# Kernel tuning notes

Hardware: AMD Instinct MI355X
Metric: run time of the kernel (lower is better)

The kernel has to match this reference:

```python
import jax, jax.numpy as jnp
import numpy as np

V, E, H, C = 30000, 128, 256, 9  # vocab, embed dim, lstm hidden, num tags
B, S = 64, 512


def setup_inputs() -> dict:
    key = jax.random.key(0)
    ks = jax.random.split(key, 16)
    rn = lambda k, shape: jax.random.normal(k, shape, jnp.float32) * 0.1
    return {
        "token_ids": jax.random.randint(ks[0], (B, S), 0, V),
        "labels": jax.random.randint(ks[1], (B, S), 0, C),
        "attention_masks": jnp.ones((B, S), jnp.int32),
        "emb": rn(ks[2], (V, E)),
        # layer 0: input E; layer 1: input 2H. dim 0 = direction (fwd, bwd)
        "w_ih0": rn(ks[3], (2, 4 * H, E)),
        "w_hh0": rn(ks[4], (2, 4 * H, H)),
        "b_ih0": rn(ks[5], (2, 4 * H)),
        "b_hh0": rn(ks[6], (2, 4 * H)),
        "w_ih1": rn(ks[7], (2, 4 * H, 2 * H)),
        "w_hh1": rn(ks[8], (2, 4 * H, H)),
        "b_ih1": rn(ks[9], (2, 4 * H)),
        "b_hh1": rn(ks[10], (2, 4 * H)),
        "cls_w": rn(ks[11], (C, 2 * H)),
        "cls_b": rn(ks[12], (C,)),
        "start_trans": rn(ks[13], (C,)),
        "end_trans": rn(ks[14], (C,)),
        "trans": rn(ks[15], (C, C)),
    }


def _lstm_dir(x, w_ih, w_hh, b_ih, b_hh, reverse):
    # x: [B,S,in] -> [B,S,H]; gate order i,f,g,o as in torch
    Bq = x.shape[0]
    Hq = w_hh.shape[1]
    xg = jnp.einsum('bsi,gi->bsg', x, w_ih) + b_ih  # [B,S,4H]

    def step(carry, xg_t):
        h, c = carry
        g = xg_t + h @ w_hh.T + b_hh
        i, f, gg, o = jnp.split(g, 4, axis=-1)
        c = jax.nn.sigmoid(f) * c + jax.nn.sigmoid(i) * jnp.tanh(gg)
        h = jax.nn.sigmoid(o) * jnp.tanh(c)
        return (h, c), h

    init = (jnp.zeros((Bq, Hq), x.dtype), jnp.zeros((Bq, Hq), x.dtype))
    _, hs = jax.lax.scan(step, init, jnp.swapaxes(xg, 0, 1), reverse=reverse)
    return jnp.swapaxes(hs, 0, 1)


def _bilstm_layer(x, w_ih, w_hh, b_ih, b_hh):
    fwd = _lstm_dir(x, w_ih[0], w_hh[0], b_ih[0], b_hh[0], False)
    bwd = _lstm_dir(x, w_ih[1], w_hh[1], b_ih[1], b_hh[1], True)
    return jnp.concatenate([fwd, bwd], axis=-1)


def _crf_llh(em, tags, mask, start, end, trans):
    # torchcrf log-likelihood; em [B,S,C], tags [B,S], mask [B,S]
    m = mask.astype(em.dtype)
    em_tag = jnp.take_along_axis(em, tags[..., None], axis=2)[..., 0]  # [B,S]
    tr = trans[tags[:, :-1], tags[:, 1:]]  # [B,S-1]
    num = start[tags[:, 0]] + em_tag[:, 0] + jnp.sum(m[:, 1:] * (tr + em_tag[:, 1:]), axis=1)
    last_idx = jnp.sum(mask, axis=1).astype(jnp.int32) - 1
    last_tag = jnp.take_along_axis(tags, last_idx[:, None], axis=1)[:, 0]
    num = num + end[last_tag]

    alpha0 = start[None, :] + em[:, 0]  # [B,C]

    def step(alpha, xs):
        em_t, m_t = xs
        nxt = jax.nn.logsumexp(alpha[:, :, None] + trans[None] + em_t[:, None, :], axis=1)
        return jnp.where(m_t[:, None] > 0, nxt, alpha), None

    xs = (jnp.swapaxes(em[:, 1:], 0, 1), jnp.swapaxes(m[:, 1:], 0, 1))
    alpha, _ = jax.lax.scan(step, alpha0, xs)
    den = jax.nn.logsumexp(alpha + end[None, :], axis=1)
    return num - den


def _viterbi(em, mask, start, end, trans):
    Cq = em.shape[2]
    m = mask > 0
    score0 = start[None, :] + em[:, 0]
    idc = jnp.arange(Cq, dtype=jnp.int32)

    def step(score, xs):
        em_t, m_t = xs
        brd = score[:, :, None] + trans[None]  # [B,C_prev,C_next]
        best_prev = jnp.argmax(brd, axis=1).astype(jnp.int32)
        nxt = jnp.max(brd, axis=1) + em_t
        new = jnp.where(m_t[:, None], nxt, score)
        bp = jnp.where(m_t[:, None], best_prev, idc[None, :])  # self-pointer past seq end
        return new, bp

    xs = (jnp.swapaxes(em[:, 1:], 0, 1), jnp.swapaxes(m[:, 1:], 0, 1))
    score, hist = jax.lax.scan(step, score0, xs)  # hist: [S-1,B,C]
    last = jnp.argmax(score + end[None, :], axis=1).astype(jnp.int32)

    def back(tag, bp_t):
        prev = jnp.take_along_axis(bp_t, tag[:, None], axis=1)[:, 0]
        return prev, prev

    _, prevs = jax.lax.scan(back, last, hist, reverse=True)  # [S-1,B]
    return jnp.concatenate([jnp.swapaxes(prevs, 0, 1), last[:, None]], axis=1)  # [B,S]


def reference(token_ids, labels, attention_masks, emb, w_ih0, w_hh0, b_ih0, b_hh0,
              w_ih1, w_hh1, b_ih1, b_hh1, cls_w, cls_b, start_trans, end_trans, trans):
    x = emb[token_ids]  # [B,S,E]
    h = _bilstm_layer(x, w_ih0, w_hh0, b_ih0, b_hh0)  # [B,S,2H] (eval mode: no dropout)
    h = _bilstm_layer(h, w_ih1, w_hh1, b_ih1, b_hh1)
    emissions = h @ cls_w.T + cls_b  # [B,S,C]
    llh = _crf_llh(emissions, labels, attention_masks, start_trans, end_trans, trans)
    loss = -jnp.mean(llh)  # reduction='mean', negated
    tags = _viterbi(emissions, attention_masks, start_trans, end_trans, trans)
    return (loss, tags)
```

## Files before the change

kernel.cpp:

```cpp
#include <hip/hip_runtime.h>
#include <math.h>

#define BB 64
#define SS 512
#define EE 128
#define HH 256
#define NC 9
#define G4 1024
#define TCLOG 7
#define TC 128
#define NCH (SS / TC)

#define KLQ 9

typedef _Float16 half2v __attribute__((ext_vector_type(2)));

__device__ __forceinline__ float sigf(float x) {
    return 1.0f / (1.0f + __expf(-x));
}
__device__ __forceinline__ float tanhfast(float x) {
    float a = fabsf(x);
    float e = __expf(-2.0f * a);
    float t = (1.0f - e) / (1.0f + e);
    return copysignf(t, x);
}
__device__ __forceinline__ float dot8h(uint4 w, uint4 h, float acc) {
    acc = __builtin_amdgcn_fdot2(__builtin_bit_cast(half2v, w.x),
                                 __builtin_bit_cast(half2v, h.x), acc, false);
    acc = __builtin_amdgcn_fdot2(__builtin_bit_cast(half2v, w.y),
                                 __builtin_bit_cast(half2v, h.y), acc, false);
    acc = __builtin_amdgcn_fdot2(__builtin_bit_cast(half2v, w.z),
                                 __builtin_bit_cast(half2v, h.z), acc, false);
    acc = __builtin_amdgcn_fdot2(__builtin_bit_cast(half2v, w.w),
                                 __builtin_bit_cast(half2v, h.w), acc, false);
    return acc;
}
__device__ __forceinline__ int dot16q(uint4 w, uint4 h, int acc) {
    acc = __builtin_amdgcn_sdot4((int)w.x, (int)h.x, acc, false);
    acc = __builtin_amdgcn_sdot4((int)w.y, (int)h.y, acc, false);
    acc = __builtin_amdgcn_sdot4((int)w.z, (int)h.z, acc, false);
    acc = __builtin_amdgcn_sdot4((int)w.w, (int)h.w, acc, false);
    return acc;
}
__device__ __forceinline__ ushort f16b(float x) {
    return __builtin_bit_cast(ushort, (_Float16)x);
}

__global__ void quant_whh(const float* __restrict__ whh, uint* __restrict__ wTq,
                          float* __restrict__ swf) {
    const int row = blockIdx.x;
    const int t = threadIdx.x;
    float4 v = *(const float4*)(whh + (long)row * 256 + t * 4);
    float mx = fmaxf(fmaxf(fabsf(v.x), fabsf(v.y)), fmaxf(fabsf(v.z), fabsf(v.w)));
    #pragma unroll
    for (int o = 32; o > 0; o >>= 1) mx = fmaxf(mx, __shfl_xor(mx, o));
    float inv = (mx > 0.f) ? 127.f / mx : 0.f;
    int q0 = (int)rintf(v.x * inv) & 255;
    int q1 = (int)rintf(v.y * inv) & 255;
    int q2 = (int)rintf(v.z * inv) & 255;
    int q3 = (int)rintf(v.w * inv) & 255;
    uint u = (uint)q0 | ((uint)q1 << 8) | ((uint)q2 << 16) | ((uint)q3 << 24);
    const int dir = row >> 10, j = row & 1023;
    const int kc = t >> 2, l4 = t & 3;
    wTq[(((long)(dir * 16 + kc) * 1024 + j) << 2) + l4] = u;
    if (t == 0) swf[row] = (mx > 0.f) ? (mx / 127.f) * (1.f / 127.f) : 0.f;
}

__global__ void quant_wih1(const float* __restrict__ w, uint* __restrict__ wq,
                           float* __restrict__ swf) {
    const int row = blockIdx.x;
    const int t = threadIdx.x;
    float4 a = *(const float4*)(w + (long)row * 512 + t * 8);
    float4 b = *(const float4*)(w + (long)row * 512 + t * 8 + 4);
    float mx = fmaxf(fmaxf(fmaxf(fabsf(a.x), fabsf(a.y)), fmaxf(fabsf(a.z), fabsf(a.w))),
                     fmaxf(fmaxf(fabsf(b.x), fabsf(b.y)), fmaxf(fabsf(b.z), fabsf(b.w))));
    #pragma unroll
    for (int o = 32; o > 0; o >>= 1) mx = fmaxf(mx, __shfl_xor(mx, o));
    float inv = (mx > 0.f) ? 127.f / mx : 0.f;
    uint q0 = (uint)((int)rintf(a.x * inv) & 255) | ((uint)((int)rintf(a.y * inv) & 255) << 8)
            | ((uint)((int)rintf(a.z * inv) & 255) << 16) | ((uint)((int)rintf(a.w * inv) & 255) << 24);
    uint q1 = (uint)((int)rintf(b.x * inv) & 255) | ((uint)((int)rintf(b.y * inv) & 255) << 8)
            | ((uint)((int)rintf(b.z * inv) & 255) << 16) | ((uint)((int)rintf(b.w * inv) & 255) << 24);
    wq[(long)row * 128 + t * 2]     = q0;
    wq[(long)row * 128 + t * 2 + 1] = q1;
    if (t == 0) swf[row] = (mx > 0.f) ? mx / (127.f * 127.f) : 0.f;
}

__global__ void pack_f16(const float* __restrict__ in, ushort* __restrict__ out, int n8) {
    int i = blockIdx.x * 256 + threadIdx.x;
    if (i >= n8) return;
    float4 a = *(const float4*)(in + (long)i * 8);
    float4 b = *(const float4*)(in + (long)i * 8 + 4);
    _Float16 o[8] = {(_Float16)a.x, (_Float16)a.y, (_Float16)a.z, (_Float16)a.w,
                     (_Float16)b.x, (_Float16)b.y, (_Float16)b.z, (_Float16)b.w};
    *(uint4*)(out + (long)i * 8) = *(uint4*)o;
}

template <int KDIM, bool GATHER>
__global__ __launch_bounds__(256, 2) void gemm_xg16b(
    const void* __restrict__ Av, const int* __restrict__ tokens,
    const ushort* __restrict__ Wh, const float* __restrict__ bias,
    float* __restrict__ out, int t_base, int t_sign)
{
    __shared__ uint4 As[2][144];
    __shared__ uint4 Bs[2][144];
    const int tid = threadIdx.x;
    const int m0 = blockIdx.x * 128;
    const int n0 = blockIdx.y * 128;

    const int lr  = tid & 127;
    const int lk8 = tid >> 7;
    const int tcc = (m0 + lr) & (TC - 1);
    const int b   = (m0 + lr) >> TCLOG;
    const int tglob = t_base + t_sign * tcc;
    const long arow = (long)b * SS + tglob;
    const float*  Af = GATHER ? ((const float*)Av + (long)tokens[arow] * KDIM + lk8 * 8) : nullptr;
    const ushort* Ah = GATHER ? nullptr : ((const ushort*)Av + arow * (long)KDIM + lk8 * 8);
    const ushort* Wp = Wh + (long)(n0 + lr) * KDIM + lk8 * 8;
    const int lpad = lr + (lr >> 3);

    const int tr = tid >> 4;
    const int tn = tid & 15;

    float acc[8][8];
    #pragma unroll
    for (int i = 0; i < 8; i++)
        #pragma unroll
        for (int j = 0; j < 8; j++) acc[i][j] = 0.f;

    #pragma unroll 1
    for (int k0 = 0; k0 < KDIM; k0 += 16) {
        uint4 aw, bw;
        if (GATHER) {
            float4 a0 = *(const float4*)(Af + k0);
            float4 a1 = *(const float4*)(Af + k0 + 4);
            aw.x = (uint)f16b(a0.x) | ((uint)f16b(a0.y) << 16);
            aw.y = (uint)f16b(a0.z) | ((uint)f16b(a0.w) << 16);
            aw.z = (uint)f16b(a1.x) | ((uint)f16b(a1.y) << 16);
            aw.w = (uint)f16b(a1.z) | ((uint)f16b(a1.w) << 16);
        } else {
            aw = *(const uint4*)(Ah + k0);
        }
        bw = *(const uint4*)(Wp + k0);
        As[lk8][lpad] = aw;
        Bs[lk8][lpad] = bw;
        __syncthreads();
        #pragma unroll
        for (int k8 = 0; k8 < 2; k8++) {
            uint4 a[8], w[8];
            #pragma unroll
            for (int i = 0; i < 8; i++) {
                a[i] = As[k8][tr * 9 + i];
                w[i] = Bs[k8][tn * 9 + i];
            }
            #pragma unroll
            for (int i = 0; i < 8; i++)
                #pragma unroll
                for (int j = 0; j < 8; j++)
                    acc[i][j] = dot8h(w[j], a[i], acc[i][j]);
        }
        __syncthreads();
    }

    float4 bc0 = *(const float4*)(bias + n0 + tn * 8);
    float4 bc1 = *(const float4*)(bias + n0 + tn * 8 + 4);
    #pragma unroll
    for (int i = 0; i < 8; i++) {
        float* op = out + (long)(m0 + tr * 8 + i) * G4 + n0 + tn * 8;
        float4 r0, r1;
        r0.x = acc[i][0] + bc0.x; r0.y = acc[i][1] + bc0.y;
        r0.z = acc[i][2] + bc0.z; r0.w = acc[i][3] + bc0.w;
        r1.x = acc[i][4] + bc1.x; r1.y = acc[i][5] + bc1.y;
        r1.z = acc[i][6] + bc1.z; r1.w = acc[i][7] + bc1.w;
        *(float4*)op = r0;
        *(float4*)(op + 4) = r1;
    }
}

__global__ __launch_bounds__(256, 2) void gemm_xg8(
    const unsigned char* __restrict__ A8,
    const uint* __restrict__ Wq,
    const float* __restrict__ swf,
    const float* __restrict__ bias,
    float* __restrict__ out,
    int t_base, int t_sign)
{
    __shared__ uint4 As[144];
    __shared__ uint4 Bs[144];
    const int tid = threadIdx.x;
    const int m0 = blockIdx.x * 128;
    const int n0 = blockIdx.y * 128;

    const int lr   = tid & 127;
    const int half = tid >> 7;
    const int tcc = (m0 + lr) & (TC - 1);
    const int b   = (m0 + lr) >> TCLOG;
    const int tglob = t_base + t_sign * tcc;
    const long arow = (long)b * SS + tglob;
    const uint4* Ap = (const uint4*)(A8 + arow * 512);
    const uint4* Wp = (const uint4*)Wq + (long)(n0 + lr) * 32;
    const int lpad = lr + (lr >> 3);

    const int tr = tid >> 4;
    const int tn = tid & 15;

    int acc[8][8];
    #pragma unroll
    for (int i = 0; i < 8; i++)
        #pragma unroll
        for (int j = 0; j < 8; j++) acc[i][j] = 0;

    #pragma unroll 1
    for (int k0 = 0; k0 < 32; k0++) {
        uint4 v = half ? Wp[k0] : Ap[k0];
        if (half) Bs[lpad] = v; else As[lpad] = v;
        __syncthreads();
        uint4 a[8], w[8];
        #pragma unroll
        for (int i = 0; i < 8; i++) {
            a[i] = As[tr * 9 + i];
            w[i] = Bs[tn * 9 + i];
        }
        #pragma unroll
        for (int i = 0; i < 8; i++)
            #pragma unroll
            for (int j = 0; j < 8; j++)
                acc[i][j] = dot16q(w[j], a[i], acc[i][j]);
        __syncthreads();
    }

    float s[8], bs[8];
    #pragma unroll
    for (int jj = 0; jj < 8; jj++) {
        s[jj]  = swf[n0 + tn * 8 + jj];
        bs[jj] = bias[n0 + tn * 8 + jj];
    }
    #pragma unroll
    for (int i = 0; i < 8; i++) {
        float r[8];
        #pragma unroll
        for (int jj = 0; jj < 8; jj++) r[jj] = fmaf((float)acc[i][jj], s[jj], bs[jj]);
        float* op = out + (long)(m0 + tr * 8 + i) * G4 + n0 + tn * 8;
        *(float4*)op       = make_float4(r[0], r[1], r[2], r[3]);
        *(float4*)(op + 4) = make_float4(r[4], r[5], r[6], r[7]);
    }
}

__global__ __launch_bounds__(1024, 4) void lstm_qscan(
    const float* __restrict__ xgF, const float* __restrict__ xgB,
    const uint* __restrict__ wTq,
    const float* __restrict__ swf,
    const float* __restrict__ bhh2,
    ushort* __restrict__ hout,
    unsigned char* __restrict__ hout8,
    int doW8,
    float* __restrict__ state,
    int tbF, int tbB, int doInit)
{
    const int b = blockIdx.x;
    const int d = blockIdx.y;
    const int j = threadIdx.x;
    const float* xg = (d ? xgB : xgF) + (long)b * TC * G4 + j;
    const uint4* wTd = (const uint4*)wTq + (long)d * 16 * 1024;

    __shared__ __align__(16) uint hq[2][64];
    __shared__ float gl[G4];
    __shared__ uint4 lwq[KLQ * 1024];

    #pragma unroll
    for (int kc = 0; kc < KLQ; kc++)
        lwq[kc * 1024 + j] = wTd[(long)kc * 1024 + j];

    const float bj  = bhh2[d * G4 + j];
    const float scl = swf[d * G4 + j];
    float c_reg = 0.f, h_reg = 0.f;
    if (j < HH) {
        if (!doInit) {
            h_reg = state[((d * BB + b) * 2 + 0) * HH + j];
            c_reg = state[((d * BB + b) * 2 + 1) * HH + j];
        }
        ((char*)hq[0])[j] = (char)__float2int_rn(h_reg * 127.f);
    }
    __syncthreads();

    #pragma unroll 1
    for (int tc = 0; tc < TC; ++tc) {
        const int rb = tc & 1;
        const uint4* hc = (const uint4*)hq[rb];
        int isum = 0;

        #pragma unroll
        for (int kc = 0; kc < KLQ; kc++)
            isum = dot16q(lwq[kc * 1024 + j], hc[kc], isum);
        #pragma unroll
        for (int kc = KLQ; kc < 16; kc++)
            isum = dot16q(wTd[(long)kc * 1024 + j], hc[kc], isum);

        gl[j] = fmaf((float)isum, scl, xg[(long)tc * G4] + bj);
        __syncthreads();
        if (j < HH) {
            float gi = gl[j], gf = gl[j + 256], gg = gl[j + 512], go = gl[j + 768];
            c_reg = sigf(gf) * c_reg + sigf(gi) * tanhfast(gg);
            float h = sigf(go) * tanhfast(c_reg);
            h_reg = h;
            int qh = __float2int_rn(h * 127.f);
            ((char*)hq[rb ^ 1])[j] = (char)qh;
            const int t = d ? (tbB - tc) : (tbF + tc);
            if (doW8) hout8[((long)(b * SS + t)) * 512 + d * HH + j] = (unsigned char)(char)qh;
            else      hout [((long)(b * SS + t)) * 512 + d * HH + j] = f16b(h);
        }
        __syncthreads();
    }

    if (j < HH) {
        state[((d * BB + b) * 2 + 0) * HH + j] = h_reg;
        state[((d * BB + b) * 2 + 1) * HH + j] = c_reg;
    }
}

__global__ __launch_bounds__(256) void emissions_k16(
    const ushort* __restrict__ h1, const float* __restrict__ clsw,
    const float* __restrict__ clsb, float* __restrict__ em)
{
    long u = (long)blockIdx.x * 256 + threadIdx.x;
    if (u >= (long)BB * SS * NC) return;
    int c = (int)(u % NC);
    long m = u / NC;
    const uint* hr = (const uint*)(h1 + m * 512);
    const float2* wr = (const float2*)(clsw + (long)c * 512);
    float s0 = 0, s1 = 0;
    #pragma unroll 8
    for (int q = 0; q < 256; q += 2) {
        half2v h0 = __builtin_bit_cast(half2v, hr[q]);
        half2v h1v = __builtin_bit_cast(half2v, hr[q + 1]);
        float2 w0 = wr[q], w1 = wr[q + 1];
        s0 += (float)h0.x * w0.x + (float)h0.y * w0.y;
        s1 += (float)h1v.x * w1.x + (float)h1v.y * w1.y;
    }
    em[u] = s0 + s1 + clsb[c];
}

__global__ __launch_bounds__(64) void crf_llh(
    const float* __restrict__ em, const int* __restrict__ labels,
    const int* __restrict__ mask, const float* __restrict__ start,
    const float* __restrict__ endt, const float* __restrict__ trans,
    float* __restrict__ llh)
{
    int b = blockIdx.x, j = threadIdx.x;
    bool act = j < NC;
    float tcol[NC];
    #pragma unroll
    for (int i = 0; i < NC; i++) tcol[i] = act ? trans[i * NC + j] : 0.f;
    const float* emb_ = em + (long)b * SS * NC;
    const int* lb = labels + b * SS;
    const int* mk = mask + b * SS;
    float alpha = act ? (start[j] + emb_[j]) : -1e30f;

    float num = 0.f;
    int msum = 0;
    for (int t = j; t < SS; t += 64) msum += (mk[t] != 0);
    for (int t = 1 + j; t < SS; t += 64) {
        float m = (float)mk[t];
        num += m * (trans[lb[t - 1] * NC + lb[t]] + emb_[t * NC + lb[t]]);
    }
    for (int o = 32; o > 0; o >>= 1) {
        num  += __shfl_down(num, o);
        msum += __shfl_down(msum, o);
    }
    msum = __shfl(msum, 0);

    for (int t = 1; t < SS; t++) {
        int m = mk[t];
        float emj = act ? emb_[t * NC + j] : 0.f;
        float v[NC];
        float mx = -1e30f;
        #pragma unroll
        for (int i = 0; i < NC; i++) {
            v[i] = __shfl(alpha, i) + tcol[i];
            mx = fmaxf(mx, v[i]);
        }
        float sum = 0.f;
        #pragma unroll
        for (int i = 0; i < NC; i++) sum += __expf(v[i] - mx);
        float nxt = mx + __logf(sum) + emj;
        if (m > 0 && act) alpha = nxt;
    }
    float fin = act ? alpha + endt[j] : -1e30f;
    float mx = -1e30f;
    #pragma unroll
    for (int i = 0; i < NC; i++) mx = fmaxf(mx, __shfl(fin, i));
    float s = 0.f;
    #pragma unroll
    for (int i = 0; i < NC; i++) s += __expf(__shfl(fin, i) - mx);
    float den = mx + __logf(s);
    if (j == 0) {
        int last_idx = msum - 1;
        float numer = num + start[lb[0]] + emb_[lb[0]] + endt[lb[last_idx]];
        llh[b] = numer - den;
    }
}

__global__ __launch_bounds__(64) void loss_k(const float* __restrict__ llh, float* __restrict__ out) {
    int j = threadIdx.x;
    float v = llh[j];
    for (int o = 32; o > 0; o >>= 1) v += __shfl_down(v, o);
    if (j == 0) out[0] = -v / 64.0f;
}

__global__ __launch_bounds__(64) void viterbi_k(
    const float* __restrict__ em, const int* __restrict__ mask,
    const float* __restrict__ start, const float* __restrict__ endt,
    const float* __restrict__ trans, float* __restrict__ outp)
{
    int b = blockIdx.x, j = threadIdx.x;
    bool act = j < NC;
    __shared__ unsigned char bp[SS][NC];
    float tcol[NC];
    #pragma unroll
    for (int i = 0; i < NC; i++) tcol[i] = act ? trans[i * NC + j] : 0.f;
    const float* emb_ = em + (long)b * SS * NC;
    const int* mk = mask + b * SS;
    float score = act ? (start[j] + emb_[j]) : -1e30f;

    for (int t = 1; t < SS; t++) {
        float best = 0.f;
        int bi = 0;
        #pragma unroll
        for (int i = 0; i < NC; i++) {
            float vv = __shfl(score, i) + tcol[i];
            if (i == 0 || vv > best) { best = vv; bi = i; }
        }
        int m = mk[t];
        float nxt = best + (act ? emb_[t * NC + j] : 0.f);
        if (act) {
            if (m > 0) { score = nxt; bp[t][j] = (unsigned char)bi; }
            else       { bp[t][j] = (unsigned char)j; }
        }
    }
    float fin = act ? score + endt[j] : -1e30f;
    float bestf = 0.f;
    int last = 0;
    #pragma unroll
    for (int i = 0; i < NC; i++) {
        float vv = __shfl(fin, i);
        if (i == 0 || vv > bestf) { bestf = vv; last = i; }
    }
    __syncthreads();
    if (j == 0) {
        int cur = last;
        outp[1 + (long)b * SS + (SS - 1)] = (float)cur;
        for (int t = SS - 1; t >= 1; t--) {
            cur = bp[t][cur];
            outp[1 + (long)b * SS + (t - 1)] = (float)cur;
        }
    }
}

extern "C" void kernel_launch(void* const* d_in, const int* in_sizes, int n_in,
                              void* d_out, int out_size, void* d_ws, size_t ws_size,
                              hipStream_t stream) {
    const int*   tok    = (const int*)d_in[0];
    const int*   lab    = (const int*)d_in[1];
    const int*   msk    = (const int*)d_in[2];
    const float* emb    = (const float*)d_in[3];
    const float* w_ih0  = (const float*)d_in[4];
    const float* w_hh0  = (const float*)d_in[5];
    const float* b_ih0  = (const float*)d_in[6];
    const float* b_hh0  = (const float*)d_in[7];
    const float* w_ih1  = (const float*)d_in[8];
    const float* w_hh1  = (const float*)d_in[9];
    const float* b_ih1  = (const float*)d_in[10];
    const float* b_hh1  = (const float*)d_in[11];
    const float* clsw   = (const float*)d_in[12];
    const float* clsb   = (const float*)d_in[13];
    const float* startt = (const float*)d_in[14];
    const float* endt   = (const float*)d_in[15];
    const float* transm = (const float*)d_in[16];
    float* out = (float*)d_out;

    size_t nH8  = (size_t)BB * SS * 512 / 4;
    size_t nHh  = (size_t)BB * SS * 512 / 2;
    size_t nWQ  = (size_t)2 * 16 * 1024 * 4;
    size_t nSW  = (size_t)2 * 1024;
    size_t nWI0 = (size_t)2048 * 128 / 2;
    size_t nWQ1 = (size_t)2048 * 128;
    size_t nEM  = (size_t)BB * SS * NC;
    size_t nST  = (size_t)2 * BB * 2 * HH;
    size_t nXG  = (size_t)BB * TC * G4;

    float* H08f = (float*)d_ws;
    float* H1f  = H08f + nH8;
    float* WQ0  = H1f + nHh;
    float* WQ1w = WQ0 + nWQ;
    float* SW0  = WQ1w + nWQ;
    float* SW1  = SW0 + nSW;
    float* WI0  = SW1 + nSW;
    float* WQI1 = WI0 + nWI0;
    float* SWI1 = WQI1 + nWQ1;
    float* EM   = SWI1 + 2048;
    float* ST   = EM + nEM;
    float* LLH  = ST + nST;
    float* XGF  = LLH + 64;
    float* XGB  = XGF + nXG;

    unsigned char* H08 = (unsigned char*)H08f;
    ushort* H1h  = (ushort*)H1f;
    ushort* WI0h = (ushort*)WI0;

    quant_whh<<<2048, 64, 0, stream>>>(w_hh0, (uint*)WQ0, SW0);
    quant_whh<<<2048, 64, 0, stream>>>(w_hh1, (uint*)WQ1w, SW1);
    quant_wih1<<<2048, 64, 0, stream>>>(w_ih1, (uint*)WQI1, SWI1);
    pack_f16<<<(2048 * 128 / 8 + 255) / 256, 256, 0, stream>>>(w_ih0, WI0h, 2048 * 128 / 8);

    dim3 gg2((BB * TC) / 128, G4 / 128);
    dim3 rg(BB, 2);

    for (int c = 0; c < NCH; c++) {
        int tbF = c * TC;
        int tbB = SS - 1 - c * TC;
        gemm_xg16b<128, true><<<gg2, 256, 0, stream>>>(emb, tok, WI0h,              b_ih0,        XGF, tbF, +1);
        gemm_xg16b<128, true><<<gg2, 256, 0, stream>>>(emb, tok, WI0h + 1024 * 128, b_ih0 + 1024, XGB, tbB, -1);
        lstm_qscan<<<rg, 1024, 0, stream>>>(XGF, XGB, (const uint*)WQ0, SW0, b_hh0,
                                            H1h, H08, 1, ST, tbF, tbB, c == 0);
    }
    for (int c = 0; c < NCH; c++) {
        int tbF = c * TC;
        int tbB = SS - 1 - c * TC;
        gemm_xg8<<<gg2, 256, 0, stream>>>(H08, (const uint*)WQI1,              SWI1,        b_ih1,        XGF, tbF, +1);
        gemm_xg8<<<gg2, 256, 0, stream>>>(H08, (const uint*)WQI1 + 1024 * 128, SWI1 + 1024, b_ih1 + 1024, XGB, tbB, -1);
        lstm_qscan<<<rg, 1024, 0, stream>>>(XGF, XGB, (const uint*)WQ1w, SW1, b_hh1,
                                            H1h, H08, 0, ST, tbF, tbB, c == 0);
    }

    emissions_k16<<<((BB * SS * NC) + 255) / 256, 256, 0, stream>>>(H1h, clsw, clsb, EM);
    crf_llh<<<BB, 64, 0, stream>>>(EM, lab, msk, startt, endt, transm, LLH);
    loss_k<<<1, 64, 0, stream>>>(LLH, out);
    viterbi_k<<<BB, 64, 0, stream>>>(EM, msk, startt, endt, transm, out);
}
```

Measured before the change: 2.249 ms.

## Fuse LSTM scan and next-chunk input GEMMs into one overlapped megakernel

New measurement: 2.195 ms. 1.02x faster.

```diff
diff --git a/kernel.cpp b/kernel.cpp
--- a/kernel.cpp
+++ b/kernel.cpp
@@ -3,7 +3,6 @@
 
 #define BB 64
 #define SS 512
-#define EE 128
 #define HH 256
 #define NC 9
 #define G4 1024
@@ -44,6 +43,223 @@
 }
 __device__ __forceinline__ ushort f16b(float x) {
     return __builtin_bit_cast(ushort, (_Float16)x);
+}
+
+struct GJob {
+    const void*  A;
+    const int*   tok;
+    const void*  W;
+    const float* sw;
+    const float* bias;
+    ushort*      out;
+    int tb, ts, is8, pad;
+};
+struct SJob {
+    const ushort* xgF; const ushort* xgB;
+    const uint*  wTq; const float* swf; const float* bhh2;
+    ushort* hout; unsigned char* hout8; float* state;
+    int doW8, tbF, tbB, doInit;
+};
+struct MegaP {
+    SJob s;
+    GJob g[4];
+    int nScan, nGemm;
+};
+
+__device__ __forceinline__ int pad4(int r) { return r + (r >> 3); }
+
+__device__ void gemm16_dev(unsigned char* sm, const GJob& G, int bx, int by) {
+    uint4* As = (uint4*)sm;
+    uint4* Bs = As + 288;
+    const int tid = threadIdx.x;
+    const int m0 = bx * 128, n0 = by * 128;
+    const int lr = tid & 127, lk8 = (tid >> 7) & 1;
+    const int lpad = lr + (lr >> 3);
+    const bool isA = tid < 256, isB = (tid >= 256 && tid < 512);
+    const int tcc = (m0 + lr) & (TC - 1);
+    const int bb  = (m0 + lr) >> TCLOG;
+    const int tglob = G.tb + G.ts * tcc;
+    const long arow = (long)bb * SS + tglob;
+    const float*  Af = isA ? ((const float*)G.A + (long)G.tok[arow] * 128 + lk8 * 8) : nullptr;
+    const ushort* Wp = isB ? ((const ushort*)G.W + (long)(n0 + lr) * 128 + lk8 * 8) : nullptr;
+    const int tr = tid >> 5, tn = tid & 31;
+
+    float acc[4][4];
+    #pragma unroll
+    for (int i = 0; i < 4; i++)
+        #pragma unroll
+        for (int j = 0; j < 4; j++) acc[i][j] = 0.f;
+
+    #pragma unroll 1
+    for (int k0 = 0; k0 < 128; k0 += 16) {
+        if (isA) {
+            float4 a0 = *(const float4*)(Af + k0);
+            float4 a1 = *(const float4*)(Af + k0 + 4);
+            uint4 aw;
+            aw.x = (uint)f16b(a0.x) | ((uint)f16b(a0.y) << 16);
+            aw.y = (uint)f16b(a0.z) | ((uint)f16b(a0.w) << 16);
+            aw.z = (uint)f16b(a1.x) | ((uint)f16b(a1.y) << 16);
+            aw.w = (uint)f16b(a1.z) | ((uint)f16b(a1.w) << 16);
+            As[lk8 * 144 + lpad] = aw;
+        } else if (isB) {
+            Bs[lk8 * 144 + lpad] = *(const uint4*)(Wp + k0);
+        }
+        __syncthreads();
+        #pragma unroll
+        for (int k8 = 0; k8 < 2; k8++) {
+            uint4 a[4], w[4];
+            #pragma unroll
+            for (int i = 0; i < 4; i++) {
+                a[i] = As[k8 * 144 + pad4(tr * 4 + i)];
+                w[i] = Bs[k8 * 144 + pad4(tn * 4 + i)];
+            }
+            #pragma unroll
+            for (int i = 0; i < 4; i++)
+                #pragma unroll
+                for (int j = 0; j < 4; j++)
+                    acc[i][j] = dot8h(w[j], a[i], acc[i][j]);
+        }
+        __syncthreads();
+    }
+
+    float4 bc = *(const float4*)(G.bias + n0 + tn * 4);
+    #pragma unroll
+    for (int i = 0; i < 4; i++) {
+        ushort4 o;
+        o.x = f16b(acc[i][0] + bc.x);
+        o.y = f16b(acc[i][1] + bc.y);
+        o.z = f16b(acc[i][2] + bc.z);
+        o.w = f16b(acc[i][3] + bc.w);
+        *(ushort4*)(G.out + (long)(m0 + tr * 4 + i) * G4 + n0 + tn * 4) = o;
+    }
+}
+
+__device__ void gemm8_dev(unsigned char* sm, const GJob& G, int bx, int by) {
+    uint4* As = (uint4*)sm;
+    uint4* Bs = As + 144;
+    const int tid = threadIdx.x;
+    const int m0 = bx * 128, n0 = by * 128;
+    const int lr = tid & 127;
+    const int lpad = lr + (lr >> 3);
+    const bool isA = tid < 128, isB = (tid >= 128 && tid < 256);
+    const int tcc = (m0 + lr) & (TC - 1);
+    const int bb  = (m0 + lr) >> TCLOG;
+    const int tglob = G.tb + G.ts * tcc;
+    const long arow = (long)bb * SS + tglob;
+    const uint4* Ap = isA ? (const uint4*)((const unsigned char*)G.A + arow * 512) : nullptr;
+    const uint4* Wp = isB ? ((const uint4*)G.W + (long)(n0 + lr) * 32) : nullptr;
+    const int tr = tid >> 5, tn = tid & 31;
+
+    int acc[4][4];
+    #pragma unroll
+    for (int i = 0; i < 4; i++)
+        #pragma unroll
+        for (int j = 0; j < 4; j++) acc[i][j] = 0;
+
+    #pragma unroll 1
+    for (int k0 = 0; k0 < 32; k0++) {
+        if (isA) As[lpad] = Ap[k0];
+        else if (isB) Bs[lpad] = Wp[k0];
+        __syncthreads();
+        uint4 a[4], w[4];
+        #pragma unroll
+        for (int i = 0; i < 4; i++) {
+            a[i] = As[pad4(tr * 4 + i)];
+            w[i] = Bs[pad4(tn * 4 + i)];
+        }
+        #pragma unroll
+        for (int i = 0; i < 4; i++)
+            #pragma unroll
+            for (int j = 0; j < 4; j++)
+                acc[i][j] = dot16q(w[j], a[i], acc[i][j]);
+        __syncthreads();
+    }
+
+    #pragma unroll
+    for (int i = 0; i < 4; i++) {
+        ushort4 o;
+        #pragma unroll
+        for (int j = 0; j < 4; j++) {
+            float r = fmaf((float)acc[i][j], G.sw[n0 + tn * 4 + j], G.bias[n0 + tn * 4 + j]);
+            ((ushort*)&o)[j] = f16b(r);
+        }
+        *(ushort4*)(G.out + (long)(m0 + tr * 4 + i) * G4 + n0 + tn * 4) = o;
+    }
+}
+
+__device__ void scan_dev(unsigned char* sm, const SJob& S, int b, int d) {
+    const int j = threadIdx.x;
+    const ushort* xg = (d ? S.xgB : S.xgF) + (long)b * TC * G4 + j;
+    const uint4* wTd = (const uint4*)S.wTq + (long)d * 16 * 1024;
+
+    uint4* lwq = (uint4*)sm;
+    float* gl  = (float*)(sm + 147456);
+    uint*  hq  = (uint*)(sm + 147456 + 4096);
+
+    #pragma unroll
+    for (int kc = 0; kc < KLQ; kc++)
+        lwq[kc * 1024 + j] = wTd[(long)kc * 1024 + j];
+
+    const float bj  = S.bhh2[d * G4 + j];
+    const float scl = S.swf[d * G4 + j];
+    float c_reg = 0.f, h_reg = 0.f;
+    if (j < HH) {
+        if (!S.doInit) {
+            h_reg = S.state[((d * BB + b) * 2 + 0) * HH + j];
+            c_reg = S.state[((d * BB + b) * 2 + 1) * HH + j];
+        }
+        ((char*)hq)[j] = (char)__float2int_rn(h_reg * 127.f);
+    }
+    __syncthreads();
+
+    #pragma unroll 1
+    for (int tc = 0; tc < TC; ++tc) {
+        const int rb = tc & 1;
+        const uint4* hc = (const uint4*)(hq + rb * 64);
+        int isum = 0;
+        #pragma unroll
+        for (int kc = 0; kc < KLQ; kc++)
+            isum = dot16q(lwq[kc * 1024 + j], hc[kc], isum);
+        #pragma unroll
+        for (int kc = KLQ; kc < 16; kc++)
+            isum = dot16q(wTd[(long)kc * 1024 + j], hc[kc], isum);
+
+        float xv = (float)__builtin_bit_cast(_Float16, xg[(long)tc * G4]);
+        gl[j] = fmaf((float)isum, scl, xv + bj);
+        __syncthreads();
+        if (j < HH) {
+            float gi = gl[j], gf = gl[j + 256], gg = gl[j + 512], go = gl[j + 768];
+            c_reg = sigf(gf) * c_reg + sigf(gi) * tanhfast(gg);
+            float h = sigf(go) * tanhfast(c_reg);
+            h_reg = h;
+            int qh = __float2int_rn(h * 127.f);
+            ((char*)(hq + (rb ^ 1) * 64))[j] = (char)qh;
+            const int t = d ? (S.tbB - tc) : (S.tbF + tc);
+            if (S.doW8) S.hout8[((long)(b * SS + t)) * 512 + d * HH + j] = (unsigned char)(char)qh;
+            else        S.hout [((long)(b * SS + t)) * 512 + d * HH + j] = f16b(h);
+        }
+        __syncthreads();
+    }
+
+    if (j < HH) {
+        S.state[((d * BB + b) * 2 + 0) * HH + j] = h_reg;
+        S.state[((d * BB + b) * 2 + 1) * HH + j] = c_reg;
+    }
+}
+
+__global__ __launch_bounds__(1024, 4) void mega(MegaP p) {
+    __shared__ __align__(16) unsigned char sm[152064];
+    const int blk = blockIdx.x;
+    if (blk < p.nScan * 128) {
+        const int local = blk & 127;
+        scan_dev(sm, p.s, local & 63, local >> 6);
+    } else {
+        const int gb = blk - p.nScan * 128;
+        const int job = gb >> 9, t = gb & 511;
+        const GJob& G = p.g[job];
+        if (G.is8) gemm8_dev(sm, G, t & 63, t >> 6);
+        else       gemm16_dev(sm, G, t & 63, t >> 6);
+    }
 }
 
 __global__ void quant_whh(const float* __restrict__ whh, uint* __restrict__ wTq,
@@ -94,228 +310,6 @@
     _Float16 o[8] = {(_Float16)a.x, (_Float16)a.y, (_Float16)a.z, (_Float16)a.w,
                      (_Float16)b.x, (_Float16)b.y, (_Float16)b.z, (_Float16)b.w};
     *(uint4*)(out + (long)i * 8) = *(uint4*)o;
-}
-
-template <int KDIM, bool GATHER>
-__global__ __launch_bounds__(256, 2) void gemm_xg16b(
-    const void* __restrict__ Av, const int* __restrict__ tokens,
-    const ushort* __restrict__ Wh, const float* __restrict__ bias,
-    float* __restrict__ out, int t_base, int t_sign)
-{
-    __shared__ uint4 As[2][144];
-    __shared__ uint4 Bs[2][144];
-    const int tid = threadIdx.x;
-    const int m0 = blockIdx.x * 128;
-    const int n0 = blockIdx.y * 128;
-
-    const int lr  = tid & 127;
-    const int lk8 = tid >> 7;
-    const int tcc = (m0 + lr) & (TC - 1);
-    const int b   = (m0 + lr) >> TCLOG;
-    const int tglob = t_base + t_sign * tcc;
-    const long arow = (long)b * SS + tglob;
-    const float*  Af = GATHER ? ((const float*)Av + (long)tokens[arow] * KDIM + lk8 * 8) : nullptr;
-    const ushort* Ah = GATHER ? nullptr : ((const ushort*)Av + arow * (long)KDIM + lk8 * 8);
-    const ushort* Wp = Wh + (long)(n0 + lr) * KDIM + lk8 * 8;
-    const int lpad = lr + (lr >> 3);
-
-    const int tr = tid >> 4;
-    const int tn = tid & 15;
-
-    float acc[8][8];
-    #pragma unroll
-    for (int i = 0; i < 8; i++)
-        #pragma unroll
-        for (int j = 0; j < 8; j++) acc[i][j] = 0.f;
-
-    #pragma unroll 1
-    for (int k0 = 0; k0 < KDIM; k0 += 16) {
-        uint4 aw, bw;
-        if (GATHER) {
-            float4 a0 = *(const float4*)(Af + k0);
-            float4 a1 = *(const float4*)(Af + k0 + 4);
-            aw.x = (uint)f16b(a0.x) | ((uint)f16b(a0.y) << 16);
-            aw.y = (uint)f16b(a0.z) | ((uint)f16b(a0.w) << 16);
-            aw.z = (uint)f16b(a1.x) | ((uint)f16b(a1.y) << 16);
-            aw.w = (uint)f16b(a1.z) | ((uint)f16b(a1.w) << 16);
-        } else {
-            aw = *(const uint4*)(Ah + k0);
-        }
-        bw = *(const uint4*)(Wp + k0);
-        As[lk8][lpad] = aw;
-        Bs[lk8][lpad] = bw;
-        __syncthreads();
-        #pragma unroll
-        for (int k8 = 0; k8 < 2; k8++) {
-            uint4 a[8], w[8];
-            #pragma unroll
-            for (int i = 0; i < 8; i++) {
-                a[i] = As[k8][tr * 9 + i];
-                w[i] = Bs[k8][tn * 9 + i];
-            }
-            #pragma unroll
-            for (int i = 0; i < 8; i++)
-                #pragma unroll
-                for (int j = 0; j < 8; j++)
-                    acc[i][j] = dot8h(w[j], a[i], acc[i][j]);
-        }
-        __syncthreads();
-    }
-
-    float4 bc0 = *(const float4*)(bias + n0 + tn * 8);
-    float4 bc1 = *(const float4*)(bias + n0 + tn * 8 + 4);
-    #pragma unroll
-    for (int i = 0; i < 8; i++) {
-        float* op = out + (long)(m0 + tr * 8 + i) * G4 + n0 + tn * 8;
-        float4 r0, r1;
-        r0.x = acc[i][0] + bc0.x; r0.y = acc[i][1] + bc0.y;
-        r0.z = acc[i][2] + bc0.z; r0.w = acc[i][3] + bc0.w;
-        r1.x = acc[i][4] + bc1.x; r1.y = acc[i][5] + bc1.y;
-        r1.z = acc[i][6] + bc1.z; r1.w = acc[i][7] + bc1.w;
-        *(float4*)op = r0;
-        *(float4*)(op + 4) = r1;
-    }
-}
-
-__global__ __launch_bounds__(256, 2) void gemm_xg8(
-    const unsigned char* __restrict__ A8,
-    const uint* __restrict__ Wq,
-    const float* __restrict__ swf,
-    const float* __restrict__ bias,
-    float* __restrict__ out,
-    int t_base, int t_sign)
-{
-    __shared__ uint4 As[144];
-    __shared__ uint4 Bs[144];
-    const int tid = threadIdx.x;
-    const int m0 = blockIdx.x * 128;
-    const int n0 = blockIdx.y * 128;
-
-    const int lr   = tid & 127;
-    const int half = tid >> 7;
-    const int tcc = (m0 + lr) & (TC - 1);
-    const int b   = (m0 + lr) >> TCLOG;
-    const int tglob = t_base + t_sign * tcc;
-    const long arow = (long)b * SS + tglob;
-    const uint4* Ap = (const uint4*)(A8 + arow * 512);
-    const uint4* Wp = (const uint4*)Wq + (long)(n0 + lr) * 32;
-    const int lpad = lr + (lr >> 3);
-
-    const int tr = tid >> 4;
-    const int tn = tid & 15;
-
-    int acc[8][8];
-    #pragma unroll
-    for (int i = 0; i < 8; i++)
-        #pragma unroll
-        for (int j = 0; j < 8; j++) acc[i][j] = 0;
-
-    #pragma unroll 1
-    for (int k0 = 0; k0 < 32; k0++) {
-        uint4 v = half ? Wp[k0] : Ap[k0];
-        if (half) Bs[lpad] = v; else As[lpad] = v;
-        __syncthreads();
-        uint4 a[8], w[8];
-        #pragma unroll
-        for (int i = 0; i < 8; i++) {
-            a[i] = As[tr * 9 + i];
-            w[i] = Bs[tn * 9 + i];
-        }
-        #pragma unroll
-        for (int i = 0; i < 8; i++)
-            #pragma unroll
-            for (int j = 0; j < 8; j++)
-                acc[i][j] = dot16q(w[j], a[i], acc[i][j]);
-        __syncthreads();
-    }
-
-    float s[8], bs[8];
-    #pragma unroll
-    for (int jj = 0; jj < 8; jj++) {
-        s[jj]  = swf[n0 + tn * 8 + jj];
-        bs[jj] = bias[n0 + tn * 8 + jj];
-    }
-    #pragma unroll
-    for (int i = 0; i < 8; i++) {
-        float r[8];
-        #pragma unroll
-        for (int jj = 0; jj < 8; jj++) r[jj] = fmaf((float)acc[i][jj], s[jj], bs[jj]);
-        float* op = out + (long)(m0 + tr * 8 + i) * G4 + n0 + tn * 8;
-        *(float4*)op       = make_float4(r[0], r[1], r[2], r[3]);
-        *(float4*)(op + 4) = make_float4(r[4], r[5], r[6], r[7]);
-    }
-}
-
-__global__ __launch_bounds__(1024, 4) void lstm_qscan(
-    const float* __restrict__ xgF, const float* __restrict__ xgB,
-    const uint* __restrict__ wTq,
-    const float* __restrict__ swf,
-    const float* __restrict__ bhh2,
-    ushort* __restrict__ hout,
-    unsigned char* __restrict__ hout8,
-    int doW8,
-    float* __restrict__ state,
-    int tbF, int tbB, int doInit)
-{
-    const int b = blockIdx.x;
-    const int d = blockIdx.y;
-    const int j = threadIdx.x;
-    const float* xg = (d ? xgB : xgF) + (long)b * TC * G4 + j;
-    const uint4* wTd = (const uint4*)wTq + (long)d * 16 * 1024;
-
-    __shared__ __align__(16) uint hq[2][64];
-    __shared__ float gl[G4];
-    __shared__ uint4 lwq[KLQ * 1024];
-
-    #pragma unroll
-    for (int kc = 0; kc < KLQ; kc++)
-        lwq[kc * 1024 + j] = wTd[(long)kc * 1024 + j];
-
-    const float bj  = bhh2[d * G4 + j];
-    const float scl = swf[d * G4 + j];
-    float c_reg = 0.f, h_reg = 0.f;
-    if (j < HH) {
-        if (!doInit) {
-            h_reg = state[((d * BB + b) * 2 + 0) * HH + j];
-            c_reg = state[((d * BB + b) * 2 + 1) * HH + j];
-        }
-        ((char*)hq[0])[j] = (char)__float2int_rn(h_reg * 127.f);
-    }
-    __syncthreads();
-
-    #pragma unroll 1
-    for (int tc = 0; tc < TC; ++tc) {
-        const int rb = tc & 1;
-        const uint4* hc = (const uint4*)hq[rb];
-        int isum = 0;
-
-        #pragma unroll
-        for (int kc = 0; kc < KLQ; kc++)
-            isum = dot16q(lwq[kc * 1024 + j], hc[kc], isum);
-        #pragma unroll
-        for (int kc = KLQ; kc < 16; kc++)
-            isum = dot16q(wTd[(long)kc * 1024 + j], hc[kc], isum);
-
-        gl[j] = fmaf((float)isum, scl, xg[(long)tc * G4] + bj);
-        __syncthreads();
-        if (j < HH) {
-            float gi = gl[j], gf = gl[j + 256], gg = gl[j + 512], go = gl[j + 768];
-            c_reg = sigf(gf) * c_reg + sigf(gi) * tanhfast(gg);
-            float h = sigf(go) * tanhfast(c_reg);
-            h_reg = h;
-            int qh = __float2int_rn(h * 127.f);
-            ((char*)hq[rb ^ 1])[j] = (char)qh;
-            const int t = d ? (tbB - tc) : (tbF + tc);
-            if (doW8) hout8[((long)(b * SS + t)) * 512 + d * HH + j] = (unsigned char)(char)qh;
-            else      hout [((long)(b * SS + t)) * 512 + d * HH + j] = f16b(h);
-        }
-        __syncthreads();
-    }
-
-    if (j < HH) {
-        state[((d * BB + b) * 2 + 0) * HH + j] = h_reg;
-        state[((d * BB + b) * 2 + 1) * HH + j] = c_reg;
-    }
 }
 
 __global__ __launch_bounds__(256) void emissions_k16(
@@ -480,17 +474,22 @@
 
     size_t nH8  = (size_t)BB * SS * 512 / 4;
     size_t nHh  = (size_t)BB * SS * 512 / 2;
+    size_t xgHalf = (size_t)BB * TC * G4;
+    size_t nXGb = xgHalf * 2 / 2;
     size_t nWQ  = (size_t)2 * 16 * 1024 * 4;
     size_t nSW  = (size_t)2 * 1024;
     size_t nWI0 = (size_t)2048 * 128 / 2;
     size_t nWQ1 = (size_t)2048 * 128;
     size_t nEM  = (size_t)BB * SS * NC;
     size_t nST  = (size_t)2 * BB * 2 * HH;
-    size_t nXG  = (size_t)BB * TC * G4;
 
     float* H08f = (float*)d_ws;
     float* H1f  = H08f + nH8;
-    float* WQ0  = H1f + nHh;
+    float* XG0a = H1f + nHh;
+    float* XG0b = XG0a + nXGb;
+    float* XG1a = XG0b + nXGb;
+    float* XG1b = XG1a + nXGb;
+    float* WQ0  = XG1b + nXGb;
     float* WQ1w = WQ0 + nWQ;
     float* SW0  = WQ1w + nWQ;
     float* SW1  = SW0 + nSW;
@@ -498,39 +497,75 @@
     float* WQI1 = WI0 + nWI0;
     float* SWI1 = WQI1 + nWQ1;
     float* EM   = SWI1 + 2048;
-    float* ST   = EM + nEM;
-    float* LLH  = ST + nST;
-    float* XGF  = LLH + 64;
-    float* XGB  = XGF + nXG;
+    float* ST0  = EM + nEM;
+    float* ST1  = ST0 + nST;
+    float* LLH  = ST1 + nST;
 
     unsigned char* H08 = (unsigned char*)H08f;
     ushort* H1h  = (ushort*)H1f;
     ushort* WI0h = (ushort*)WI0;
+    ushort* XG0[2] = {(ushort*)XG0a, (ushort*)XG0b};
+    ushort* XG1[2] = {(ushort*)XG1a, (ushort*)XG1b};
 
     quant_whh<<<2048, 64, 0, stream>>>(w_hh0, (uint*)WQ0, SW0);
     quant_whh<<<2048, 64, 0, stream>>>(w_hh1, (uint*)WQ1w, SW1);
     quant_wih1<<<2048, 64, 0, stream>>>(w_ih1, (uint*)WQI1, SWI1);
     pack_f16<<<(2048 * 128 / 8 + 255) / 256, 256, 0, stream>>>(w_ih0, WI0h, 2048 * 128 / 8);
 
-    dim3 gg2((BB * TC) / 128, G4 / 128);
-    dim3 rg(BB, 2);
-
-    for (int c = 0; c < NCH; c++) {
-        int tbF = c * TC;
-        int tbB = SS - 1 - c * TC;
-        gemm_xg16b<128, true><<<gg2, 256, 0, stream>>>(emb, tok, WI0h,              b_ih0,        XGF, tbF, +1);
-        gemm_xg16b<128, true><<<gg2, 256, 0, stream>>>(emb, tok, WI0h + 1024 * 128, b_ih0 + 1024, XGB, tbB, -1);
-        lstm_qscan<<<rg, 1024, 0, stream>>>(XGF, XGB, (const uint*)WQ0, SW0, b_hh0,
-                                            H1h, H08, 1, ST, tbF, tbB, c == 0);
-    }
-    for (int c = 0; c < NCH; c++) {
-        int tbF = c * TC;
-        int tbB = SS - 1 - c * TC;
-        gemm_xg8<<<gg2, 256, 0, stream>>>(H08, (const uint*)WQI1,              SWI1,        b_ih1,        XGF, tbF, +1);
-        gemm_xg8<<<gg2, 256, 0, stream>>>(H08, (const uint*)WQI1 + 1024 * 128, SWI1 + 1024, b_ih1 + 1024, XGB, tbB, -1);
-        lstm_qscan<<<rg, 1024, 0, stream>>>(XGF, XGB, (const uint*)WQ1w, SW1, b_hh1,
-                                            H1h, H08, 0, ST, tbF, tbB, c == 0);
-    }
+    auto g16 = [&](int c, int dd) {
+        GJob g{};
+        g.A = emb; g.tok = tok;
+        g.W = WI0h + (size_t)dd * 1024 * 128;
+        g.sw = nullptr; g.bias = b_ih0 + dd * 1024;
+        g.out = XG0[c & 1] + (size_t)dd * xgHalf;
+        g.tb = dd ? (SS - 1 - c * TC) : (c * TC);
+        g.ts = dd ? -1 : 1;
+        g.is8 = 0;
+        return g;
+    };
+    auto g8 = [&](int c, int dd) {
+        GJob g{};
+        g.A = H08; g.tok = nullptr;
+        g.W = (const uint*)WQI1 + (size_t)dd * 1024 * 128;
+        g.sw = SWI1 + dd * 1024; g.bias = b_ih1 + dd * 1024;
+        g.out = XG1[c & 1] + (size_t)dd * xgHalf;
+        g.tb = dd ? (SS - 1 - c * TC) : (c * TC);
+        g.ts = dd ? -1 : 1;
+        g.is8 = 1;
+        return g;
+    };
+    auto sj = [&](int layer, int c) {
+        SJob s{};
+        ushort* xgb = layer ? XG1[c & 1] : XG0[c & 1];
+        s.xgF = xgb; s.xgB = xgb + xgHalf;
+        s.wTq = (const uint*)(layer ? WQ1w : WQ0);
+        s.swf = layer ? SW1 : SW0;
+        s.bhh2 = layer ? b_hh1 : b_hh0;
+        s.hout = H1h; s.hout8 = H08;
+        s.doW8 = layer ? 0 : 1;
+        s.state = layer ? ST1 : ST0;
+        s.tbF = c * TC; s.tbB = SS - 1 - c * TC;
+        s.doInit = (c == 0);
+        return s;
+    };
+    auto launch = [&](int nS, SJob s, GJob* gj, int nG) {
+        MegaP p{};
+        p.s = s;
+        for (int i = 0; i < nG; i++) p.g[i] = gj[i];
+        p.nScan = nS; p.nGemm = nG;
+        mega<<<nS * 128 + nG * 512, 1024, 0, stream>>>(p);
+    };
+
+    { GJob j2[2] = {g16(0, 0), g16(0, 1)};        launch(0, SJob{}, j2, 2); }
+    { GJob j2[2] = {g16(1, 0), g16(1, 1)};        launch(1, sj(0, 0), j2, 2); }
+    { GJob j2[2] = {g16(2, 0), g16(2, 1)};        launch(1, sj(0, 1), j2, 2); }
+    { GJob j2[2] = {g16(3, 0), g16(3, 1)};        launch(1, sj(0, 2), j2, 2); }
+    {                                              launch(1, sj(0, 3), nullptr, 0); }
+    { GJob j4[4] = {g8(0, 0), g8(0, 1), g8(1, 0), g8(1, 1)}; launch(0, SJob{}, j4, 4); }
+    {                                              launch(1, sj(1, 0), nullptr, 0); }
+    { GJob j2[2] = {g8(2, 0), g8(2, 1)};          launch(1, sj(1, 1), j2, 2); }
+    { GJob j2[2] = {g8(3, 0), g8(3, 1)};          launch(1, sj(1, 2), j2, 2); }
+    {                                              launch(1, sj(1, 3), nullptr, 0); }
 
     emissions_k16<<<((BB * SS * NC) + 255) / 256, 256, 0, stream>>>(H1h, clsw, clsb, EM);
     crf_llh<<<BB, 64, 0, stream>>>(EM, lab, msk, startt, endt, transm, LLH);
```
